# Performance work log

Hardware: AMD Instinct MI355X
Metric: run time of the kernel (lower is better)

Reference implementation:

```python
import jax, jax.numpy as jnp
import numpy as np

B, S, N, D, M = 8, 8192, 16, 64, 64
EPS = 1e-6

def _elu_feature_map(x):
    # elu(x) + 1
    return jax.nn.elu(x) + 1.0

def setup_inputs() -> dict:
    key = jax.random.key(0)
    k1, k2, k3, k4 = jax.random.split(key, 4)
    query = jax.random.normal(k1, (B, N, D), dtype=jnp.float32)
    key_t = jax.random.normal(k2, (B, S, N, D), dtype=jnp.float32)
    value = jax.random.normal(k3, (B, S, N, M), dtype=jnp.float32)
    key_mask = jax.random.randint(k4, (B, S), 0, 2).astype(bool)
    return {"query": query, "key": key_t, "value": value, "key_mask": key_mask}

def reference(query, key, value, key_mask):
    # feature maps: elu(x)+1
    Q = _elu_feature_map(query)                 # [b, n, d]
    K = _elu_feature_map(key)                   # [b, s, n, d]
    # mask True -> zero out keys (masked_fill semantics)
    K = jnp.where(key_mask[:, :, None, None], 0.0, K)
    # accumulate K (outer) V state over sequence
    Sst = jnp.einsum('bsnd,bsnm->bnmd', K, value)   # [b, n, m, d]
    Z = K.sum(axis=1)                               # [b, n, d]
    QZ = 1.0 / (jnp.einsum('bnd,bnd->bn', Q, Z) + EPS)  # [b, n]
    V = jnp.einsum('bnd,bnmd,bn->bnm', Q, Sst, QZ)      # [b, n, m]
    return V, Sst, Z
```

## Files before the change

### kernel.cpp

```cpp
#include <hip/hip_runtime.h>
#include <hip/hip_bf16.h>
#include <stdint.h>

#define BB 8
#define SS 8192
#define NN 16
#define DD 64
#define MM 64
#define TS 32
#define PAD 40

typedef __attribute__((ext_vector_type(8))) short bf16x8;
typedef __attribute__((ext_vector_type(4))) float f32x4;

__device__ __forceinline__ float feat(float x) {
    return x > 0.0f ? (x + 1.0f) : __expf(x);
}

__device__ __forceinline__ uint32_t bf16bits(float x) {
    __hip_bfloat16 h = __float2bfloat16(x);
    return (uint32_t)*reinterpret_cast<unsigned short*>(&h);
}

__device__ __forceinline__ int swz_col(int row, int oct, int within) {
    return ((oct ^ ((row >> 2) & 3)) << 3) + within;
}

__global__ __launch_bounds__(256)
void rcla_partial(const float* __restrict__ key,
                  const float* __restrict__ value,
                  const int* __restrict__ mask,
                  float* __restrict__ ws, int C) {
    const int blk = blockIdx.x;
    const int c  = blk % C;
    const int bn = blk / C;
    const int b  = bn >> 4;
    const int n  = bn & 15;
    const int t  = threadIdx.x;

    const int a  = t & 15;
    const int p  = t >> 4;
    const int c0 = a << 2;
    const int sl = p << 1;

    const int lane = t & 63;
    const int w    = t >> 6;
    const int wm   = (w >> 1) << 5;
    const int wd   = (w & 1) << 5;
    const int g    = lane >> 4;
    const int lr   = lane & 15;

    __shared__ __align__(16) __hip_bfloat16 Kl[2][DD][PAD];
    __shared__ __align__(16) __hip_bfloat16 Vl[2][MM][PAD];

    const int steps   = SS / C;
    const int nt      = steps / TS;
    const int s_begin = c * steps;

    const float* kb = key   + (((size_t)b * SS) * NN + n) * DD + (size_t)s_begin * (NN * DD);
    const float* vb = value + (((size_t)b * SS) * NN + n) * MM + (size_t)s_begin * (NN * MM);
    const int*   mb = mask  + (size_t)b * SS + s_begin;

    uint64_t bits = 0;
    for (int i = 0; i < nt; ++i) {
        bits |= (uint64_t)(mb[i * TS + sl]     != 0) << (2 * i);
        bits |= (uint64_t)(mb[i * TS + sl + 1] != 0) << (2 * i + 1);
    }

    f32x4 acc[2][2] = {};
    float zacc[4] = {0.f, 0.f, 0.f, 0.f};

    const float4 z4 = make_float4(0.f, 0.f, 0.f, 0.f);
    float4 kq0 = z4, kq1 = z4, vq0 = z4, vq1 = z4;
    bool lv0 = false, lv1 = false;

    #define LOADT(ti)                                                                 \
        do {                                                                          \
            lv0 = !((bits >> (2 * (ti))) & 1);                                        \
            lv1 = !((bits >> (2 * (ti) + 1)) & 1);                                    \
            kq0 = z4; kq1 = z4; vq0 = z4; vq1 = z4;                                   \
            const size_t s0 = (size_t)((ti) * TS + sl);                               \
            if (lv0) {                                                                \
                kq0 = *reinterpret_cast<const float4*>(kb + s0 * (NN * DD) + c0);     \
                vq0 = *reinterpret_cast<const float4*>(vb + s0 * (NN * MM) + c0);     \
            }                                                                         \
            if (lv1) {                                                                \
                kq1 = *reinterpret_cast<const float4*>(kb + (s0+1) * (NN * DD) + c0); \
                vq1 = *reinterpret_cast<const float4*>(vb + (s0+1) * (NN * MM) + c0); \
            }                                                                         \
        } while (0)

    LOADT(0);

    const int soct = sl >> 3;
    const int swin = sl & 7;

    for (int ti = 0; ti < nt; ++ti) {
        const int buf = ti & 1;
        {
            const float k0[4] = {kq0.x, kq0.y, kq0.z, kq0.w};
            const float k1[4] = {kq1.x, kq1.y, kq1.z, kq1.w};
            const float v0[4] = {vq0.x, vq0.y, vq0.z, vq0.w};
            const float v1[4] = {vq1.x, vq1.y, vq1.z, vq1.w};
            #pragma unroll
            for (int j = 0; j < 4; ++j) {
                const float fk0 = lv0 ? feat(k0[j]) : 0.f;
                const float fk1 = lv1 ? feat(k1[j]) : 0.f;
                const float fv0 = lv0 ? v0[j] : 0.f;
                const float fv1 = lv1 ? v1[j] : 0.f;
                zacc[j] += fk0 + fk1;
                const uint32_t pk = (bf16bits(fk1) << 16) | bf16bits(fk0);
                const uint32_t pv = (bf16bits(fv1) << 16) | bf16bits(fv0);
                const int row = c0 + j;
                const int col = swz_col(row, soct, swin);
                *reinterpret_cast<uint32_t*>(&Kl[buf][row][col]) = pk;
                *reinterpret_cast<uint32_t*>(&Vl[buf][row][col]) = pv;
            }
        }

        __syncthreads();

        if (ti + 1 < nt) LOADT(ti + 1);

        const int rA0 = wm + lr, rA1 = wm + 16 + lr;
        const int rB0 = wd + lr, rB1 = wd + 16 + lr;
        const bf16x8 a0 = *reinterpret_cast<const bf16x8*>(&Vl[buf][rA0][swz_col(rA0, g, 0)]);
        const bf16x8 a1 = *reinterpret_cast<const bf16x8*>(&Vl[buf][rA1][swz_col(rA1, g, 0)]);
        const bf16x8 b0 = *reinterpret_cast<const bf16x8*>(&Kl[buf][rB0][swz_col(rB0, g, 0)]);
        const bf16x8 b1 = *reinterpret_cast<const bf16x8*>(&Kl[buf][rB1][swz_col(rB1, g, 0)]);
        acc[0][0] = __builtin_amdgcn_mfma_f32_16x16x32_bf16(a0, b0, acc[0][0], 0, 0, 0);
        acc[0][1] = __builtin_amdgcn_mfma_f32_16x16x32_bf16(a0, b1, acc[0][1], 0, 0, 0);
        acc[1][0] = __builtin_amdgcn_mfma_f32_16x16x32_bf16(a1, b0, acc[1][0], 0, 0, 0);
        acc[1][1] = __builtin_amdgcn_mfma_f32_16x16x32_bf16(a1, b1, acc[1][1], 0, 0, 0);
    }
    #undef LOADT

    float* out = ws + ((size_t)bn * C + c) * 4160;

    #pragma unroll
    for (int i = 0; i < 2; ++i)
        #pragma unroll
        for (int j = 0; j < 2; ++j)
            #pragma unroll
            for (int r = 0; r < 4; ++r) {
                const int m = wm + 16 * i + g * 4 + r;
                const int d = wd + 16 * j + lr;
                out[m * DD + d] = acc[i][j][r];
            }

    __syncthreads();
    float* Zf = reinterpret_cast<float*>(&Kl[0][0][0]);
    *reinterpret_cast<float4*>(&Zf[p * DD + c0]) =
        make_float4(zacc[0], zacc[1], zacc[2], zacc[3]);
    __syncthreads();
    if (t < DD) {
        float z = 0.f;
        #pragma unroll
        for (int q = 0; q < 16; ++q) z += Zf[q * DD + t];
        out[4096 + t] = z;
    }
}

__global__ __launch_bounds__(256)
void rcla_final(const float* __restrict__ query,
                const float* __restrict__ ws, int C,
                float* __restrict__ outV, float* __restrict__ outS,
                float* __restrict__ outZ) {
    const int q   = blockIdx.x & 3;
    const int bn  = blockIdx.x >> 2;
    const int t   = threadIdx.x;
    const int d0  = (t & 15) << 2;
    const int mr  = (q << 4) + (t >> 4);
    const float* p0 = ws + (size_t)bn * C * 4160;

    float sst[4] = {0.f, 0.f, 0.f, 0.f};
    float z[4]   = {0.f, 0.f, 0.f, 0.f};

    for (int c = 0; c < C; ++c) {
        const float* p = p0 + (size_t)c * 4160;
        const float4 v = *reinterpret_cast<const float4*>(p + mr * DD + d0);
        sst[0] += v.x; sst[1] += v.y; sst[2] += v.z; sst[3] += v.w;
        const float4 zv = *reinterpret_cast<const float4*>(p + 4096 + d0);
        z[0] += zv.x; z[1] += zv.y; z[2] += zv.z; z[3] += zv.w;
    }

    *reinterpret_cast<float4*>(outS + (size_t)bn * 4096 + mr * DD + d0) =
        make_float4(sst[0], sst[1], sst[2], sst[3]);
    if (q == 0 && t < 16) {
        *reinterpret_cast<float4*>(outZ + (size_t)bn * DD + d0) =
            make_float4(z[0], z[1], z[2], z[3]);
    }

    float qf[4];
    #pragma unroll
    for (int j = 0; j < 4; ++j) qf[j] = feat(query[(size_t)bn * DD + d0 + j]);

    float pd = qf[0]*z[0] + qf[1]*z[1] + qf[2]*z[2] + qf[3]*z[3];
    float pv = qf[0]*sst[0] + qf[1]*sst[1] + qf[2]*sst[2] + qf[3]*sst[3];
    #pragma unroll
    for (int off = 1; off < 16; off <<= 1) {
        pd += __shfl_xor(pd, off);
        pv += __shfl_xor(pv, off);
    }
    if ((t & 15) == 0) {
        const float qz = 1.0f / (pd + 1e-6f);
        outV[(size_t)bn * MM + mr] = qz * pv;
    }
}

extern "C" void kernel_launch(void* const* d_in, const int* in_sizes, int n_in,
                              void* d_out, int out_size, void* d_ws, size_t ws_size,
                              hipStream_t stream) {
    const float* query = (const float*)d_in[0];
    const float* key   = (const float*)d_in[1];
    const float* value = (const float*)d_in[2];
    const int*   mask  = (const int*)d_in[3];

    float* out  = (float*)d_out;
    float* outV = out;
    float* outS = out + BB * NN * MM;
    float* outZ = outS + BB * NN * MM * DD;
    float* ws   = (float*)d_ws;

    int C = 16;
    while (C > 8 && (size_t)BB * NN * C * 4160 * sizeof(float) > ws_size) C >>= 1;

    rcla_partial<<<dim3(BB * NN * C), dim3(256), 0, stream>>>(key, value, mask, ws, C);
    rcla_final<<<dim3(BB * NN * 4), dim3(256), 0, stream>>>(query, ws, C, outV, outS, outZ);
}
```

Measured before the change: 77.12 us.

## Deepen register prefetch to two tiles and use a lightweight LDS barrier

Result: faster. 71.01 us (-7.9%).

```diff
diff --git a/kernel.cpp b/kernel.cpp
--- a/kernel.cpp
+++ b/kernel.cpp
@@ -22,8 +22,72 @@
     return (uint32_t)*reinterpret_cast<unsigned short*>(&h);
 }
 
-__device__ __forceinline__ int swz_col(int row, int oct, int within) {
-    return ((oct ^ ((row >> 2) & 3)) << 3) + within;
+#define SYNCW()                                        \
+    do {                                               \
+        __builtin_amdgcn_sched_barrier(0);             \
+        asm volatile("s_waitcnt lgkmcnt(0)");          \
+        __builtin_amdgcn_s_barrier();                  \
+        __builtin_amdgcn_sched_barrier(0);             \
+    } while (0)
+
+struct Slot {
+    float4 kq0, kq1, vq0, vq1;
+    bool lv0, lv1;
+};
+
+__device__ __forceinline__ void load_tile(Slot& s, int ti, uint32_t bits,
+                                          const float* kb, const float* vb,
+                                          int sl, int c0) {
+    const float4 z4 = make_float4(0.f, 0.f, 0.f, 0.f);
+    s.lv0 = !((bits >> (2 * ti)) & 1);
+    s.lv1 = !((bits >> (2 * ti + 1)) & 1);
+    s.kq0 = z4; s.kq1 = z4; s.vq0 = z4; s.vq1 = z4;
+    const size_t s0 = (size_t)(ti * TS + sl);
+    if (s.lv0) {
+        s.kq0 = *reinterpret_cast<const float4*>(kb + s0 * (NN * DD) + c0);
+        s.vq0 = *reinterpret_cast<const float4*>(vb + s0 * (NN * MM) + c0);
+    }
+    if (s.lv1) {
+        s.kq1 = *reinterpret_cast<const float4*>(kb + (s0 + 1) * (NN * DD) + c0);
+        s.vq1 = *reinterpret_cast<const float4*>(vb + (s0 + 1) * (NN * MM) + c0);
+    }
+}
+
+__device__ __forceinline__ void stage_tile(const Slot& s, float* zacc,
+                                           __hip_bfloat16 (*Kbuf)[PAD],
+                                           __hip_bfloat16 (*Vbuf)[PAD],
+                                           int c0, int sl) {
+    const float sk0[4] = {s.kq0.x, s.kq0.y, s.kq0.z, s.kq0.w};
+    const float sk1[4] = {s.kq1.x, s.kq1.y, s.kq1.z, s.kq1.w};
+    const float sv0[4] = {s.vq0.x, s.vq0.y, s.vq0.z, s.vq0.w};
+    const float sv1[4] = {s.vq1.x, s.vq1.y, s.vq1.z, s.vq1.w};
+    #pragma unroll
+    for (int j = 0; j < 4; ++j) {
+        const float fk0 = s.lv0 ? feat(sk0[j]) : 0.f;
+        const float fk1 = s.lv1 ? feat(sk1[j]) : 0.f;
+        const float fv0 = s.lv0 ? sv0[j] : 0.f;
+        const float fv1 = s.lv1 ? sv1[j] : 0.f;
+        zacc[j] += fk0 + fk1;
+        const uint32_t pk = (bf16bits(fk1) << 16) | bf16bits(fk0);
+        const uint32_t pv = (bf16bits(fv1) << 16) | bf16bits(fv0);
+        *reinterpret_cast<uint32_t*>(&Kbuf[c0 + j][sl]) = pk;
+        *reinterpret_cast<uint32_t*>(&Vbuf[c0 + j][sl]) = pv;
+    }
+}
+
+__device__ __forceinline__ void mfma_step(const __hip_bfloat16 (*Kbuf)[PAD],
+                                          const __hip_bfloat16 (*Vbuf)[PAD],
+                                          f32x4& acc00, f32x4& acc01,
+                                          f32x4& acc10, f32x4& acc11,
+                                          int wm, int wd, int g, int lr) {
+    const bf16x8 fa0 = *reinterpret_cast<const bf16x8*>(&Vbuf[wm + lr][g * 8]);
+    const bf16x8 fa1 = *reinterpret_cast<const bf16x8*>(&Vbuf[wm + 16 + lr][g * 8]);
+    const bf16x8 fb0 = *reinterpret_cast<const bf16x8*>(&Kbuf[wd + lr][g * 8]);
+    const bf16x8 fb1 = *reinterpret_cast<const bf16x8*>(&Kbuf[wd + 16 + lr][g * 8]);
+    acc00 = __builtin_amdgcn_mfma_f32_16x16x32_bf16(fa0, fb0, acc00, 0, 0, 0);
+    acc01 = __builtin_amdgcn_mfma_f32_16x16x32_bf16(fa0, fb1, acc01, 0, 0, 0);
+    acc10 = __builtin_amdgcn_mfma_f32_16x16x32_bf16(fa1, fb0, acc10, 0, 0, 0);
+    acc11 = __builtin_amdgcn_mfma_f32_16x16x32_bf16(fa1, fb1, acc11, 0, 0, 0);
 }
 
 __global__ __launch_bounds__(256)
@@ -61,92 +125,40 @@
     const float* vb = value + (((size_t)b * SS) * NN + n) * MM + (size_t)s_begin * (NN * MM);
     const int*   mb = mask  + (size_t)b * SS + s_begin;
 
-    uint64_t bits = 0;
+    uint32_t bits = 0;
     for (int i = 0; i < nt; ++i) {
-        bits |= (uint64_t)(mb[i * TS + sl]     != 0) << (2 * i);
-        bits |= (uint64_t)(mb[i * TS + sl + 1] != 0) << (2 * i + 1);
-    }
-
-    f32x4 acc[2][2] = {};
+        bits |= (uint32_t)(mb[i * TS + sl]     != 0) << (2 * i);
+        bits |= (uint32_t)(mb[i * TS + sl + 1] != 0) << (2 * i + 1);
+    }
+
+    f32x4 acc00 = {}, acc01 = {}, acc10 = {}, acc11 = {};
     float zacc[4] = {0.f, 0.f, 0.f, 0.f};
 
-    const float4 z4 = make_float4(0.f, 0.f, 0.f, 0.f);
-    float4 kq0 = z4, kq1 = z4, vq0 = z4, vq1 = z4;
-    bool lv0 = false, lv1 = false;
-
-    #define LOADT(ti)                                                                 \
-        do {                                                                          \
-            lv0 = !((bits >> (2 * (ti))) & 1);                                        \
-            lv1 = !((bits >> (2 * (ti) + 1)) & 1);                                    \
-            kq0 = z4; kq1 = z4; vq0 = z4; vq1 = z4;                                   \
-            const size_t s0 = (size_t)((ti) * TS + sl);                               \
-            if (lv0) {                                                                \
-                kq0 = *reinterpret_cast<const float4*>(kb + s0 * (NN * DD) + c0);     \
-                vq0 = *reinterpret_cast<const float4*>(vb + s0 * (NN * MM) + c0);     \
-            }                                                                         \
-            if (lv1) {                                                                \
-                kq1 = *reinterpret_cast<const float4*>(kb + (s0+1) * (NN * DD) + c0); \
-                vq1 = *reinterpret_cast<const float4*>(vb + (s0+1) * (NN * MM) + c0); \
-            }                                                                         \
-        } while (0)
-
-    LOADT(0);
-
-    const int soct = sl >> 3;
-    const int swin = sl & 7;
-
-    for (int ti = 0; ti < nt; ++ti) {
-        const int buf = ti & 1;
-        {
-            const float k0[4] = {kq0.x, kq0.y, kq0.z, kq0.w};
-            const float k1[4] = {kq1.x, kq1.y, kq1.z, kq1.w};
-            const float v0[4] = {vq0.x, vq0.y, vq0.z, vq0.w};
-            const float v1[4] = {vq1.x, vq1.y, vq1.z, vq1.w};
-            #pragma unroll
-            for (int j = 0; j < 4; ++j) {
-                const float fk0 = lv0 ? feat(k0[j]) : 0.f;
-                const float fk1 = lv1 ? feat(k1[j]) : 0.f;
-                const float fv0 = lv0 ? v0[j] : 0.f;
-                const float fv1 = lv1 ? v1[j] : 0.f;
-                zacc[j] += fk0 + fk1;
-                const uint32_t pk = (bf16bits(fk1) << 16) | bf16bits(fk0);
-                const uint32_t pv = (bf16bits(fv1) << 16) | bf16bits(fv0);
-                const int row = c0 + j;
-                const int col = swz_col(row, soct, swin);
-                *reinterpret_cast<uint32_t*>(&Kl[buf][row][col]) = pk;
-                *reinterpret_cast<uint32_t*>(&Vl[buf][row][col]) = pv;
-            }
-        }
-
-        __syncthreads();
-
-        if (ti + 1 < nt) LOADT(ti + 1);
-
-        const int rA0 = wm + lr, rA1 = wm + 16 + lr;
-        const int rB0 = wd + lr, rB1 = wd + 16 + lr;
-        const bf16x8 a0 = *reinterpret_cast<const bf16x8*>(&Vl[buf][rA0][swz_col(rA0, g, 0)]);
-        const bf16x8 a1 = *reinterpret_cast<const bf16x8*>(&Vl[buf][rA1][swz_col(rA1, g, 0)]);
-        const bf16x8 b0 = *reinterpret_cast<const bf16x8*>(&Kl[buf][rB0][swz_col(rB0, g, 0)]);
-        const bf16x8 b1 = *reinterpret_cast<const bf16x8*>(&Kl[buf][rB1][swz_col(rB1, g, 0)]);
-        acc[0][0] = __builtin_amdgcn_mfma_f32_16x16x32_bf16(a0, b0, acc[0][0], 0, 0, 0);
-        acc[0][1] = __builtin_amdgcn_mfma_f32_16x16x32_bf16(a0, b1, acc[0][1], 0, 0, 0);
-        acc[1][0] = __builtin_amdgcn_mfma_f32_16x16x32_bf16(a1, b0, acc[1][0], 0, 0, 0);
-        acc[1][1] = __builtin_amdgcn_mfma_f32_16x16x32_bf16(a1, b1, acc[1][1], 0, 0, 0);
-    }
-    #undef LOADT
+    Slot sA, sB;
+    load_tile(sA, 0, bits, kb, vb, sl, c0);
+    load_tile(sB, 1, bits, kb, vb, sl, c0);
+
+    for (int ti = 0; ti < nt; ti += 2) {
+        stage_tile(sA, zacc, Kl[0], Vl[0], c0, sl);
+        if (ti + 2 < nt) load_tile(sA, ti + 2, bits, kb, vb, sl, c0);
+        SYNCW();
+        mfma_step(Kl[0], Vl[0], acc00, acc01, acc10, acc11, wm, wd, g, lr);
+
+        stage_tile(sB, zacc, Kl[1], Vl[1], c0, sl);
+        if (ti + 3 < nt) load_tile(sB, ti + 3, bits, kb, vb, sl, c0);
+        SYNCW();
+        mfma_step(Kl[1], Vl[1], acc00, acc01, acc10, acc11, wm, wd, g, lr);
+    }
 
     float* out = ws + ((size_t)bn * C + c) * 4160;
 
     #pragma unroll
-    for (int i = 0; i < 2; ++i)
-        #pragma unroll
-        for (int j = 0; j < 2; ++j)
-            #pragma unroll
-            for (int r = 0; r < 4; ++r) {
-                const int m = wm + 16 * i + g * 4 + r;
-                const int d = wd + 16 * j + lr;
-                out[m * DD + d] = acc[i][j][r];
-            }
+    for (int r = 0; r < 4; ++r) {
+        out[(wm + g * 4 + r) * DD + wd + lr]           = acc00[r];
+        out[(wm + g * 4 + r) * DD + wd + 16 + lr]      = acc01[r];
+        out[(wm + 16 + g * 4 + r) * DD + wd + lr]      = acc10[r];
+        out[(wm + 16 + g * 4 + r) * DD + wd + 16 + lr] = acc11[r];
+    }
 
     __syncthreads();
     float* Zf = reinterpret_cast<float*>(&Kl[0][0][0]);
```
